# Kernel optimization log

Measured on AMD Instinct MI355X. Metric: run time of the kernel, lower is better.

## Reference

```python
import jax, jax.numpy as jnp
import numpy as np

N = 50000          # nodes (cells)
G = 1000           # input genes
E = 800000         # edges
HIDDEN = 128
HEADS = 8
C_HID = HIDDEN // HEADS   # 16 per-head channels
LATENT = 16
NEG_SLOPE = 0.2


def _gat_layer(x, src, dst, W, a_src, a_dst, b, heads, out_ch, concat):
    """PyG GATConv (shared lin for src/dst, add_self_loops=False, eval mode)."""
    n = x.shape[0]
    h = (x @ W).reshape(n, heads, out_ch)                 # [N,H,C]
    al_s = jnp.einsum('nhc,hc->nh', h, a_src)             # [N,H]
    al_d = jnp.einsum('nhc,hc->nh', h, a_dst)             # [N,H]
    logits = jax.nn.leaky_relu(al_s[src] + al_d[dst], NEG_SLOPE)  # [E,H]
    # segment softmax over destination neighborhoods
    m = jax.ops.segment_max(logits, dst, num_segments=n)  # [N,H]
    m = jnp.where(jnp.isfinite(m), m, 0.0)                # empty segments -> 0
    e = jnp.exp(logits - m[dst])                          # [E,H]
    denom = jax.ops.segment_sum(e, dst, num_segments=n)   # [N,H]
    alpha = e / (denom[dst] + 1e-16)                      # [E,H]
    msg = h[src] * alpha[:, :, None]                      # [E,H,C]
    out = jax.ops.segment_sum(msg, dst, num_segments=n)   # [N,H,C]
    out = out.reshape(n, heads * out_ch) if concat else out.mean(axis=1)
    return out + b


def setup_inputs() -> dict:
    key = jax.random.key(0)
    ks = jax.random.split(key, 16)
    x = jax.random.normal(ks[0], (N, G), dtype=jnp.float32)
    edge_index = jax.random.randint(ks[1], (2, E), 0, N, dtype=jnp.int64)

    def glorot(k, shape):
        fan_in, fan_out = shape[0], shape[-1]
        s = jnp.sqrt(6.0 / (fan_in + fan_out)).astype(jnp.float32)
        return jax.random.uniform(k, shape, jnp.float32, -s, s)

    # layer 0: G -> 8 heads x 16 (concat -> 128)
    W0 = glorot(ks[2], (G, HEADS * C_HID))
    as0 = glorot(ks[3], (HEADS, C_HID))
    ad0 = glorot(ks[4], (HEADS, C_HID))
    b0 = jnp.zeros((HEADS * C_HID,), jnp.float32)
    # layer 1: 128 -> 8 heads x 16 (concat -> 128)
    W1 = glorot(ks[5], (HIDDEN, HEADS * C_HID))
    as1 = glorot(ks[6], (HEADS, C_HID))
    ad1 = glorot(ks[7], (HEADS, C_HID))
    b1 = jnp.zeros((HEADS * C_HID,), jnp.float32)
    # layer 2: 128 -> 1 head x 16 (concat=False -> 16)
    W2 = glorot(ks[8], (HIDDEN, LATENT))
    as2 = glorot(ks[9], (1, LATENT))
    ad2 = glorot(ks[10], (1, LATENT))
    b2 = jnp.zeros((LATENT,), jnp.float32)

    return {"x": x, "edge_index": edge_index,
            "W0": W0, "as0": as0, "ad0": ad0, "b0": b0,
            "W1": W1, "as1": as1, "ad1": ad1, "b1": b1,
            "W2": W2, "as2": as2, "ad2": ad2, "b2": b2}


def reference(x, edge_index, W0, as0, ad0, b0, W1, as1, ad1, b1, W2, as2, ad2, b2):
    src, dst = edge_index[0], edge_index[1]
    h = _gat_layer(x, src, dst, W0, as0, ad0, b0, HEADS, C_HID, concat=True)
    h = jax.nn.elu(h)
    h = _gat_layer(h, src, dst, W1, as1, ad1, b1, HEADS, C_HID, concat=True)
    h = jax.nn.elu(h)
    z = _gat_layer(h, src, dst, W2, as2, ad2, b2, 1, LATENT, concat=False)
    return z
```

## Files before the change

kernel.cpp:

```cpp
#include <hip/hip_runtime.h>
#include <hip/hip_bf16.h>
#include <math.h>

#define GENES 1000

typedef __attribute__((ext_vector_type(8))) _Float16 half8;
typedef __attribute__((ext_vector_type(4))) float f32x4;
typedef __attribute__((ext_vector_type(4))) unsigned int uint4v;
typedef __attribute__((ext_vector_type(2))) unsigned int uint2v;

__device__ inline float f16lo(unsigned int v) {
  return (float)__builtin_bit_cast(_Float16, (unsigned short)(v & 0xffffu));
}
__device__ inline float f16hi(unsigned int v) {
  return (float)__builtin_bit_cast(_Float16, (unsigned short)(v >> 16));
}


__global__ void k_deg(const int* __restrict__ ei, int* __restrict__ deg, int E) {
  int e = blockIdx.x * blockDim.x + threadIdx.x;
  if (e < E) atomicAdd(&deg[ei[E + e]], 1);
}

__global__ void k_scan1(int* __restrict__ deg, int* __restrict__ ptr,
                        int* __restrict__ bsum, int n) {
  __shared__ int ws[4];
  int t = threadIdx.x, b = blockIdx.x;
  int i = b * 256 + t;
  int lane = t & 63, w = t >> 6;
  int x = 0;
  if (i < n) { x = deg[i]; deg[i] = 0; }
  #pragma unroll
  for (int d = 1; d < 64; d <<= 1) {
    int y = __shfl_up(x, d);
    if (lane >= d) x += y;
  }
  if (lane == 63) ws[w] = x;
  __syncthreads();
  if (t == 0) {
    int s = 0;
    #pragma unroll
    for (int k = 0; k < 4; ++k) { s += ws[k]; ws[k] = s; }
  }
  __syncthreads();
  int incl = x + (w ? ws[w - 1] : 0);
  if (i < n) ptr[i + 1] = incl;
  if (t == 255) bsum[b] = incl;
  if (i == 0) ptr[0] = 0;
}

__global__ void k_scan2(int* __restrict__ bsum, int nb) {
  __shared__ int ws[4];
  int t = threadIdx.x;
  int lane = t & 63, w = t >> 6;
  int v = (t < nb) ? bsum[t] : 0;
  int x = v;
  #pragma unroll
  for (int d = 1; d < 64; d <<= 1) {
    int y = __shfl_up(x, d);
    if (lane >= d) x += y;
  }
  if (lane == 63) ws[w] = x;
  __syncthreads();
  if (t == 0) {
    int s = 0;
    #pragma unroll
    for (int k = 0; k < 4; ++k) { s += ws[k]; ws[k] = s; }
  }
  __syncthreads();
  int incl = x + (w ? ws[w - 1] : 0);
  if (t < nb) bsum[t] = incl - v;
}

__global__ void k_scan3(int* __restrict__ ptr, const int* __restrict__ bsum, int n) {
  int i = blockIdx.x * 256 + threadIdx.x;
  if (i < n) ptr[i + 1] += bsum[blockIdx.x];
}

__global__ void k_scatter(const int* __restrict__ ei, const int* __restrict__ ptr,
                          int* __restrict__ cur, int* __restrict__ srcs, int E) {
  int e = blockIdx.x * blockDim.x + threadIdx.x;
  if (e >= E) return;
  int d = ei[E + e];
  int pos = ptr[d] + atomicAdd(&cur[d], 1);
  srcs[pos] = ei[e];
}


__global__ void k_wpackall(const float* __restrict__ W0, const float* __restrict__ W1,
                           const float* __restrict__ W2, unsigned short* __restrict__ P,
                           int K0) {
  int t = blockIdx.x * blockDim.x + threadIdx.x;
  if (t >= 163840) return;
  const float* W; int K, N, e;
  if (t < 131072)      { W = W0; K = K0;  N = 128; e = t; }
  else if (t < 147456) { W = W1; K = 128; N = 128; e = t - 131072; }
  else                 { W = W2; K = 128; N = 16;  e = t - 147456; }
  int s = e >> 12, rem = e & 4095;
  int q = rem >> 10, col = (rem >> 3) & 127, j = rem & 7;
  int k = s * 32 + q * 8 + j;
  float v = (k < K && col < N) ? W[(long)k * N + col] : 0.f;
  _Float16 h = (_Float16)v;
  P[t] = __builtin_bit_cast(unsigned short, h);
}


template<int HH, int NST, bool AF16, bool OF16>
__global__ __launch_bounds__(512) void k_mgemm8(
    const void* __restrict__ Ap, const unsigned short* __restrict__ Pb,
    void* __restrict__ outp, float* __restrict__ als, float* __restrict__ ald,
    const float* __restrict__ avs, const float* __restrict__ avd,
    int M, int K, int ldc) {
  __shared__ __align__(16) char lds[24576];
  char* bA0 = lds;
  char* bA1 = lds + 4096;
  char* bB0 = lds + 8192;
  char* bB1 = lds + 16384;

  int t = threadIdx.x, lane = t & 63;
  int r15 = lane & 15, q = lane >> 4;
  int wv = t >> 6;
  int wr = wv >> 1, wc = wv & 1;
  long row0 = (long)blockIdx.x * 64;

  int srow = t >> 3, sseg = t & 7;
  long arow = row0 + srow; if (arow >= M) arow = M - 1;
  const float* pa32 = (const float*)Ap + arow * (long)K;
  const unsigned short* pa16 = (const unsigned short*)Ap + arow * (long)K;

  f32x4 acc[4];
  #pragma unroll
  for (int nt = 0; nt < 4; ++nt) acc[nt] = (f32x4){0.f, 0.f, 0.f, 0.f};

  uint4v aA0, aA1, aA2;
  uint2v aH0, aH1, aH2;
  uint4v rB0, rB1;

  auto loadA = [&](int s, uint4v& r32, uint2v& r16) {
    int k0 = s * 32 + sseg * 4;
    if constexpr (AF16) {
      r16 = (k0 < K) ? *(const uint2v*)(pa16 + k0) : (uint2v){0u, 0u};
    } else {
      r32 = (k0 < K) ? *(const uint4v*)(pa32 + k0) : (uint4v){0u, 0u, 0u, 0u};
    }
  };
  auto writeA = [&](char* buf, uint4v r32, uint2v r16) {
    char* p = buf + ((sseg >> 1) * 1024 + srow * 16 + (sseg & 1) * 8);
    if constexpr (AF16) {
      *(uint2v*)p = r16;
    } else {
      float4 f = __builtin_bit_cast(float4, r32);
      uint2v h;
      h[0] = __builtin_bit_cast(unsigned int, __builtin_amdgcn_cvt_pkrtz(f.x, f.y));
      h[1] = __builtin_bit_cast(unsigned int, __builtin_amdgcn_cvt_pkrtz(f.z, f.w));
      *(uint2v*)p = h;
    }
  };
  auto ldA3 = [&](int tile) {
    int sl = tile % 3;
    if (sl == 0) loadA(tile, aA0, aH0);
    else if (sl == 1) loadA(tile, aA1, aH1);
    else loadA(tile, aA2, aH2);
  };
  auto wrA3 = [&](char* buf, int tile) {
    int sl = tile % 3;
    if (sl == 0) writeA(buf, aA0, aH0);
    else if (sl == 1) writeA(buf, aA1, aH1);
    else writeA(buf, aA2, aH2);
  };
  auto loadB = [&](int s, uint4v& r) {
    r = *(const uint4v*)(Pb + (size_t)s * 4096 + t * 8);
  };
  auto writeB = [&](char* buf, uint4v r) {
    *(uint4v*)(buf + t * 16) = r;
  };
  auto compute = [&](const char* bA, const char* bB) {
    half8 af = *(const half8*)(bA + q * 1024 + (wr * 16 + r15) * 16);
    #pragma unroll
    for (int nt = 0; nt < 4; ++nt) {
      half8 bf = *(const half8*)(bB + q * 2048 + (wc * 64 + nt * 16 + r15) * 16);
      acc[nt] = __builtin_amdgcn_mfma_f32_16x16x32_f16(af, bf, acc[nt], 0, 0, 0);
    }
  };

  ldA3(0); loadB(0, rB0);
  ldA3(1); loadB(1, rB1);
  ldA3(2);
  wrA3(bA0, 0); writeB(bB0, rB0);
  __syncthreads();

  #pragma unroll
  for (int s = 0; s < NST; s += 2) {
    if (s + 3 < NST) ldA3(s + 3);
    if (s + 2 < NST) loadB(s + 2, rB0);
    compute(bA0, bB0);
    if (s + 1 < NST) { wrA3(bA1, s + 1); writeB(bB1, rB1); }
    __syncthreads();
    if (s + 1 < NST) {
      if (s + 4 < NST) ldA3(s + 4);
      if (s + 3 < NST) loadB(s + 3, rB1);
      compute(bA1, bB1);
      if (s + 2 < NST) { wrA3(bA0, s + 2); writeB(bB0, rB0); }
      __syncthreads();
    }
  }

  long rbase = row0 + wr * 16 + q * 4;
  if constexpr (OF16) {
    unsigned short* o16 = (unsigned short*)outp;
    #pragma unroll
    for (int i = 0; i < 4; ++i) {
      long r = rbase + i;
      if (r < M) {
        #pragma unroll
        for (int nt = 0; nt < 4; ++nt) {
          int col = wc * 64 + nt * 16 + r15;
          _Float16 hv = (_Float16)acc[nt][i];
          o16[r * ldc + col] = __builtin_bit_cast(unsigned short, hv);
        }
      }
    }
  } else {
    float* o32 = (float*)outp;
    #pragma unroll
    for (int i = 0; i < 4; ++i) {
      long r = rbase + i;
      if (r < M) {
        #pragma unroll
        for (int nt = 0; nt < 4; ++nt) {
          int col = wc * 64 + nt * 16 + r15;
          if (col < ldc) o32[r * ldc + col] = acc[nt][i];
        }
      }
    }
  }
  #pragma unroll
  for (int nt = 0; nt < 4; ++nt) {
    int head = wc * 4 + nt;
    if (head < HH) {
      float cs = avs[head * 16 + r15];
      float cd = avd[head * 16 + r15];
      #pragma unroll
      for (int i = 0; i < 4; ++i) {
        float s1 = acc[nt][i] * cs;
        float s2 = acc[nt][i] * cd;
        #pragma unroll
        for (int d = 1; d < 16; d <<= 1) {
          s1 += __shfl_xor(s1, d);
          s2 += __shfl_xor(s2, d);
        }
        if (r15 == 0) {
          long r = rbase + i;
          if (r < M) { als[r * HH + head] = s1; ald[r * HH + head] = s2; }
        }
      }
    }
  }
}


__global__ void k_agg128h(const unsigned short* __restrict__ h,
                          const float* __restrict__ als, const float* __restrict__ ald,
                          const int* __restrict__ ptr, const int* __restrict__ srcs,
                          const float* __restrict__ bias,
                          unsigned short* __restrict__ out, int n) {
  int wid = (int)(((long)blockIdx.x * blockDim.x + threadIdx.x) >> 6);
  if (wid >= n) return;
  int lane = threadIdx.x & 63;
  int half = lane >> 5, l5 = lane & 31;
  int c0 = 4 * l5;
  int hB = l5 >> 2;
  int p0 = ptr[wid], deg = ptr[wid + 1] - p0;
  float aldB = ald[wid * 8 + hB];
  float a0 = 0.f, a1 = 0.f, a2 = 0.f, a3 = 0.f, dsum = 0.f;
  int j = half;
  for (; j + 6 < deg; j += 8) {
    int s0 = srcs[p0 + j],     s1 = srcs[p0 + j + 2];
    int s2 = srcs[p0 + j + 4], s3 = srcs[p0 + j + 6];
    float l0 = als[s0 * 8 + hB] + aldB;
    float l1 = als[s1 * 8 + hB] + aldB;
    float l2 = als[s2 * 8 + hB] + aldB;
    float l3 = als[s3 * 8 + hB] + aldB;
    uint2v h0 = *(const uint2v*)(h + (long)s0 * 128 + c0);
    uint2v h1 = *(const uint2v*)(h + (long)s1 * 128 + c0);
    uint2v h2 = *(const uint2v*)(h + (long)s2 * 128 + c0);
    uint2v h3 = *(const uint2v*)(h + (long)s3 * 128 + c0);
    l0 = l0 > 0.f ? l0 : 0.2f * l0;
    l1 = l1 > 0.f ? l1 : 0.2f * l1;
    l2 = l2 > 0.f ? l2 : 0.2f * l2;
    l3 = l3 > 0.f ? l3 : 0.2f * l3;
    float e0 = __expf(l0), e1 = __expf(l1), e2 = __expf(l2), e3 = __expf(l3);
    dsum += e0 + e1 + e2 + e3;
    a0 += e0 * f16lo(h0[0]) + e1 * f16lo(h1[0]) + e2 * f16lo(h2[0]) + e3 * f16lo(h3[0]);
    a1 += e0 * f16hi(h0[0]) + e1 * f16hi(h1[0]) + e2 * f16hi(h2[0]) + e3 * f16hi(h3[0]);
    a2 += e0 * f16lo(h0[1]) + e1 * f16lo(h1[1]) + e2 * f16lo(h2[1]) + e3 * f16lo(h3[1]);
    a3 += e0 * f16hi(h0[1]) + e1 * f16hi(h1[1]) + e2 * f16hi(h2[1]) + e3 * f16hi(h3[1]);
  }
  for (; j < deg; j += 2) {
    int s = srcs[p0 + j];
    float l = als[s * 8 + hB] + aldB;
    l = l > 0.f ? l : 0.2f * l;
    float e = __expf(l);
    uint2v hv = *(const uint2v*)(h + (long)s * 128 + c0);
    dsum += e;
    a0 += e * f16lo(hv[0]);
    a1 += e * f16hi(hv[0]);
    a2 += e * f16lo(hv[1]);
    a3 += e * f16hi(hv[1]);
  }
  a0 += __shfl_xor(a0, 32);
  a1 += __shfl_xor(a1, 32);
  a2 += __shfl_xor(a2, 32);
  a3 += __shfl_xor(a3, 32);
  dsum += __shfl_xor(dsum, 32);
  if (half == 0) {
    float inv = 1.f / (dsum + 1e-16f);
    float o0 = a0 * inv + bias[c0];
    float o1 = a1 * inv + bias[c0 + 1];
    float o2 = a2 * inv + bias[c0 + 2];
    float o3 = a3 * inv + bias[c0 + 3];
    o0 = o0 > 0.f ? o0 : (__expf(o0) - 1.f);
    o1 = o1 > 0.f ? o1 : (__expf(o1) - 1.f);
    o2 = o2 > 0.f ? o2 : (__expf(o2) - 1.f);
    o3 = o3 > 0.f ? o3 : (__expf(o3) - 1.f);
    uint2v po;
    po[0] = __builtin_bit_cast(unsigned int, __builtin_amdgcn_cvt_pkrtz(o0, o1));
    po[1] = __builtin_bit_cast(unsigned int, __builtin_amdgcn_cvt_pkrtz(o2, o3));
    *(uint2v*)(out + (long)wid * 128 + c0) = po;
  }
}


__global__ void k_agg16(const float* __restrict__ h, const float* __restrict__ als,
                        const float* __restrict__ ald, const int* __restrict__ ptr,
                        const int* __restrict__ srcs, const float* __restrict__ bias,
                        float* __restrict__ out, int n, int lda) {
  int wid = (int)(((long)blockIdx.x * blockDim.x + threadIdx.x) >> 6);
  if (wid >= n) return;
  int lane = threadIdx.x & 63;
  int p0 = ptr[wid], deg = ptr[wid + 1] - p0;
  float aldv = ald[wid];
  int g = lane >> 4, c = lane & 15;
  float acc = 0.f, dsum = 0.f;
  int j = g;
  for (; j + 12 < deg; j += 16) {
    int s0 = srcs[p0 + j],     s1 = srcs[p0 + j + 4];
    int s2 = srcs[p0 + j + 8], s3 = srcs[p0 + j + 12];
    float l0 = als[s0] + aldv, l1 = als[s1] + aldv;
    float l2 = als[s2] + aldv, l3 = als[s3] + aldv;
    float h0 = h[(long)s0 * lda + c], h1 = h[(long)s1 * lda + c];
    float h2 = h[(long)s2 * lda + c], h3 = h[(long)s3 * lda + c];
    l0 = l0 > 0.f ? l0 : 0.2f * l0;
    l1 = l1 > 0.f ? l1 : 0.2f * l1;
    l2 = l2 > 0.f ? l2 : 0.2f * l2;
    l3 = l3 > 0.f ? l3 : 0.2f * l3;
    float e0 = __expf(l0), e1 = __expf(l1), e2 = __expf(l2), e3 = __expf(l3);
    dsum += e0 + e1 + e2 + e3;
    acc += e0 * h0 + e1 * h1 + e2 * h2 + e3 * h3;
  }
  for (; j < deg; j += 4) {
    int s = srcs[p0 + j];
    float l = als[s] + aldv;
    l = l > 0.f ? l : 0.2f * l;
    float e = __expf(l);
    dsum += e;
    acc += e * h[(long)s * lda + c];
  }
  #pragma unroll
  for (int d = 16; d < 64; d <<= 1) {
    acc += __shfl_xor(acc, d);
    dsum += __shfl_xor(dsum, d);
  }
  if (lane < 16)
    out[(long)wid * 16 + lane] = acc / (dsum + 1e-16f) + bias[lane];
}


extern "C" void kernel_launch(void* const* d_in, const int* in_sizes, int n_in,
                              void* d_out, int out_size, void* d_ws, size_t ws_size,
                              hipStream_t stream) {
  const float* x  = (const float*)d_in[0];
  const int*   ei = (const int*)d_in[1];
  const float* W0 = (const float*)d_in[2];
  const float* as0= (const float*)d_in[3];
  const float* ad0= (const float*)d_in[4];
  const float* b0 = (const float*)d_in[5];
  const float* W1 = (const float*)d_in[6];
  const float* as1= (const float*)d_in[7];
  const float* ad1= (const float*)d_in[8];
  const float* b1 = (const float*)d_in[9];
  const float* W2 = (const float*)d_in[10];
  const float* as2= (const float*)d_in[11];
  const float* ad2= (const float*)d_in[12];
  const float* b2 = (const float*)d_in[13];
  float* out = (float*)d_out;

  int E = in_sizes[1] / 2;
  int n = in_sizes[0] / GENES;

  char* ws = (char*)d_ws;
  size_t off = 0;
  auto alloc = [&](size_t bytes) {
    void* p = ws + off;
    off = (off + bytes + 255) & ~(size_t)255;
    return p;
  };
  int* ptr   = (int*)alloc((size_t)(n + 1) * sizeof(int));
  int* cur   = (int*)alloc((size_t)n * sizeof(int));
  int* bsum  = (int*)alloc(512 * sizeof(int));
  int* srcs  = (int*)alloc((size_t)E * sizeof(int));
  unsigned short* Ah = (unsigned short*)alloc((size_t)n * 128 * sizeof(unsigned short));
  unsigned short* Bh = (unsigned short*)alloc((size_t)n * 128 * sizeof(unsigned short));
  float* A2  = (float*)alloc((size_t)n * 16 * sizeof(float));
  float* als = (float*)alloc((size_t)n * 8 * sizeof(float));
  float* ald = (float*)alloc((size_t)n * 8 * sizeof(float));
  unsigned short* P = (unsigned short*)alloc((size_t)163840 * sizeof(unsigned short));
  unsigned short* P0 = P;
  unsigned short* P1 = P + 131072;
  unsigned short* P2 = P + 147456;

  int eb = (E + 255) / 256;
  int nb = (n + 255) / 256;
  hipMemsetAsync(cur, 0, (size_t)n * sizeof(int), stream);
  k_deg<<<eb, 256, 0, stream>>>(ei, cur, E);
  k_scan1<<<nb, 256, 0, stream>>>(cur, ptr, bsum, n);
  k_scan2<<<1, 256, 0, stream>>>(bsum, nb);
  k_scan3<<<nb, 256, 0, stream>>>(ptr, bsum, n);
  k_scatter<<<eb, 256, 0, stream>>>(ei, ptr, cur, srcs, E);
  k_wpackall<<<640, 256, 0, stream>>>(W0, W1, W2, P, GENES);

  int mgb  = (n + 63) / 64;
  int aggb = (int)(((long)n * 64 + 255) / 256);

  k_mgemm8<8, 32, false, true><<<mgb, 512, 0, stream>>>(
      x, P0, Ah, als, ald, as0, ad0, n, GENES, 128);
  k_agg128h<<<aggb, 256, 0, stream>>>(Ah, als, ald, ptr, srcs, b0, Bh, n);

  k_mgemm8<8, 4, true, true><<<mgb, 512, 0, stream>>>(
      Bh, P1, Ah, als, ald, as1, ad1, n, 128, 128);
  k_agg128h<<<aggb, 256, 0, stream>>>(Ah, als, ald, ptr, srcs, b1, Bh, n);

  k_mgemm8<1, 4, true, false><<<mgb, 512, 0, stream>>>(
      Bh, P2, A2, als, ald, as2, ad2, n, 128, 16);
  k_agg16<<<aggb, 256, 0, stream>>>(A2, als, ald, ptr, srcs, b2, out, n, 16);
}
```

Before: 275.8 us.

## Load GEMM A fragments straight from global into registers, bypassing LDS

The GEMM kernel now loads each lane's A-operand fragment directly from global memory into registers and converts it to fp16 in place. The A tiles are no longer staged through shared memory, and only B tiles stay double-buffered in LDS. The loop now advances one K-step per iteration and uses a custom barrier that waits only on LDS counters, which removes the A LDS writes and reads and shrinks shared memory. In exchange it drops the k<K bounds check on A: the padded K tail reads past each row, into the next row or past the end of the buffer. This relies on the zero-padded packed weights to cancel those values.

Result: slower. 282.0 us (+2.2%).

```diff
diff --git a/kernel.cpp b/kernel.cpp
--- a/kernel.cpp
+++ b/kernel.cpp
@@ -14,6 +14,17 @@
 }
 __device__ inline float f16hi(unsigned int v) {
   return (float)__builtin_bit_cast(_Float16, (unsigned short)(v >> 16));
+}
+__device__ inline unsigned int pk(float a, float b) {
+  return __builtin_bit_cast(unsigned int, __builtin_amdgcn_cvt_pkrtz(a, b));
+}
+
+__device__ inline void lds_barrier() {
+  __builtin_amdgcn_sched_barrier(0);
+  asm volatile("s_waitcnt lgkmcnt(0)" ::: "memory");
+  __builtin_amdgcn_sched_barrier(0);
+  __builtin_amdgcn_s_barrier();
+  __builtin_amdgcn_sched_barrier(0);
 }
 
 
@@ -106,16 +117,12 @@
 
 
 template<int HH, int NST, bool AF16, bool OF16>
-__global__ __launch_bounds__(512) void k_mgemm8(
+__global__ __launch_bounds__(512) void k_mgemm10(
     const void* __restrict__ Ap, const unsigned short* __restrict__ Pb,
     void* __restrict__ outp, float* __restrict__ als, float* __restrict__ ald,
     const float* __restrict__ avs, const float* __restrict__ avd,
     int M, int K, int ldc) {
-  __shared__ __align__(16) char lds[24576];
-  char* bA0 = lds;
-  char* bA1 = lds + 4096;
-  char* bB0 = lds + 8192;
-  char* bB1 = lds + 16384;
+  __shared__ __align__(16) char lds[16384];
 
   int t = threadIdx.x, lane = t & 63;
   int r15 = lane & 15, q = lane >> 4;
@@ -123,85 +130,73 @@
   int wr = wv >> 1, wc = wv & 1;
   long row0 = (long)blockIdx.x * 64;
 
-  int srow = t >> 3, sseg = t & 7;
-  long arow = row0 + srow; if (arow >= M) arow = M - 1;
-  const float* pa32 = (const float*)Ap + arow * (long)K;
-  const unsigned short* pa16 = (const unsigned short*)Ap + arow * (long)K;
+  long arow = row0 + wr * 16 + r15; if (arow >= M) arow = M - 1;
+  const float* pa32 = (const float*)Ap + arow * (long)K + q * 8;
+  const unsigned short* pa16 = (const unsigned short*)Ap + arow * (long)K + q * 8;
+  const char* pB = (const char*)Pb + t * 16;
 
   f32x4 acc[4];
   #pragma unroll
   for (int nt = 0; nt < 4; ++nt) acc[nt] = (f32x4){0.f, 0.f, 0.f, 0.f};
 
-  uint4v aA0, aA1, aA2;
-  uint2v aH0, aH1, aH2;
-  uint4v rB0, rB1;
-
-  auto loadA = [&](int s, uint4v& r32, uint2v& r16) {
-    int k0 = s * 32 + sseg * 4;
+  uint4v a0lo, a0hi, a1lo, a1hi;
+  uint4v bs0, bs1;
+
+  auto issueA = [&](int s, int slot) {
     if constexpr (AF16) {
-      r16 = (k0 < K) ? *(const uint2v*)(pa16 + k0) : (uint2v){0u, 0u};
+      if (slot == 0) a0lo = *(const uint4v*)(pa16 + s * 32);
+      else           a1lo = *(const uint4v*)(pa16 + s * 32);
     } else {
-      r32 = (k0 < K) ? *(const uint4v*)(pa32 + k0) : (uint4v){0u, 0u, 0u, 0u};
+      if (slot == 0) {
+        a0lo = *(const uint4v*)(pa32 + s * 32);
+        a0hi = *(const uint4v*)(pa32 + s * 32 + 4);
+      } else {
+        a1lo = *(const uint4v*)(pa32 + s * 32);
+        a1hi = *(const uint4v*)(pa32 + s * 32 + 4);
+      }
     }
   };
-  auto writeA = [&](char* buf, uint4v r32, uint2v r16) {
-    char* p = buf + ((sseg >> 1) * 1024 + srow * 16 + (sseg & 1) * 8);
+  auto issueB = [&](int s, int slot) {
+    if (slot == 0) bs0 = *(const uint4v*)(pB + (size_t)s * 8192);
+    else           bs1 = *(const uint4v*)(pB + (size_t)s * 8192);
+  };
+  auto writeB = [&](int buf, int slot) {
+    *(uint4v*)(lds + buf * 8192 + t * 16) = (slot == 0) ? bs0 : bs1;
+  };
+  auto mkfrag = [&](int slot) -> half8 {
     if constexpr (AF16) {
-      *(uint2v*)p = r16;
+      return __builtin_bit_cast(half8, slot == 0 ? a0lo : a1lo);
     } else {
-      float4 f = __builtin_bit_cast(float4, r32);
-      uint2v h;
-      h[0] = __builtin_bit_cast(unsigned int, __builtin_amdgcn_cvt_pkrtz(f.x, f.y));
-      h[1] = __builtin_bit_cast(unsigned int, __builtin_amdgcn_cvt_pkrtz(f.z, f.w));
-      *(uint2v*)p = h;
+      float4 lo = __builtin_bit_cast(float4, slot == 0 ? a0lo : a1lo);
+      float4 hi = __builtin_bit_cast(float4, slot == 0 ? a0hi : a1hi);
+      uint4v au;
+      au[0] = pk(lo.x, lo.y); au[1] = pk(lo.z, lo.w);
+      au[2] = pk(hi.x, hi.y); au[3] = pk(hi.z, hi.w);
+      return __builtin_bit_cast(half8, au);
     }
   };
-  auto ldA3 = [&](int tile) {
-    int sl = tile % 3;
-    if (sl == 0) loadA(tile, aA0, aH0);
-    else if (sl == 1) loadA(tile, aA1, aH1);
-    else loadA(tile, aA2, aH2);
-  };
-  auto wrA3 = [&](char* buf, int tile) {
-    int sl = tile % 3;
-    if (sl == 0) writeA(buf, aA0, aH0);
-    else if (sl == 1) writeA(buf, aA1, aH1);
-    else writeA(buf, aA2, aH2);
-  };
-  auto loadB = [&](int s, uint4v& r) {
-    r = *(const uint4v*)(Pb + (size_t)s * 4096 + t * 8);
-  };
-  auto writeB = [&](char* buf, uint4v r) {
-    *(uint4v*)(buf + t * 16) = r;
-  };
-  auto compute = [&](const char* bA, const char* bB) {
-    half8 af = *(const half8*)(bA + q * 1024 + (wr * 16 + r15) * 16);
+
+  issueB(0, 0);
+  if (NST > 1) issueB(1, 1);
+  issueA(0, 0);
+  writeB(0, 0);
+  lds_barrier();
+
+  #pragma unroll
+  for (int s = 0; s < NST; ++s) {
+    const int sl = s & 1;
+    if (s + 2 < NST) issueB(s + 2, sl);
+    if (s + 1 < NST) issueA(s + 1, (s + 1) & 1);
+    half8 af = mkfrag(sl);
     #pragma unroll
     for (int nt = 0; nt < 4; ++nt) {
-      half8 bf = *(const half8*)(bB + q * 2048 + (wc * 64 + nt * 16 + r15) * 16);
+      half8 bf = *(const half8*)(lds + sl * 8192 + q * 2048 +
+                                 (wc * 64 + nt * 16 + r15) * 16);
       acc[nt] = __builtin_amdgcn_mfma_f32_16x16x32_f16(af, bf, acc[nt], 0, 0, 0);
     }
-  };
-
-  ldA3(0); loadB(0, rB0);
-  ldA3(1); loadB(1, rB1);
-  ldA3(2);
-  wrA3(bA0, 0); writeB(bB0, rB0);
-  __syncthreads();
-
-  #pragma unroll
-  for (int s = 0; s < NST; s += 2) {
-    if (s + 3 < NST) ldA3(s + 3);
-    if (s + 2 < NST) loadB(s + 2, rB0);
-    compute(bA0, bB0);
-    if (s + 1 < NST) { wrA3(bA1, s + 1); writeB(bB1, rB1); }
-    __syncthreads();
     if (s + 1 < NST) {
-      if (s + 4 < NST) ldA3(s + 4);
-      if (s + 3 < NST) loadB(s + 3, rB1);
-      compute(bA1, bB1);
-      if (s + 2 < NST) { wrA3(bA0, s + 2); writeB(bB0, rB0); }
-      __syncthreads();
+      writeB((s + 1) & 1, (s + 1) & 1);
+      lds_barrier();
     }
   }
 
@@ -432,15 +427,15 @@
   int mgb  = (n + 63) / 64;
   int aggb = (int)(((long)n * 64 + 255) / 256);
 
-  k_mgemm8<8, 32, false, true><<<mgb, 512, 0, stream>>>(
+  k_mgemm10<8, 32, false, true><<<mgb, 512, 0, stream>>>(
       x, P0, Ah, als, ald, as0, ad0, n, GENES, 128);
   k_agg128h<<<aggb, 256, 0, stream>>>(Ah, als, ald, ptr, srcs, b0, Bh, n);
 
-  k_mgemm8<8, 4, true, true><<<mgb, 512, 0, stream>>>(
+  k_mgemm10<8, 4, true, true><<<mgb, 512, 0, stream>>>(
       Bh, P1, Ah, als, ald, as1, ad1, n, 128, 128);
   k_agg128h<<<aggb, 256, 0, stream>>>(Ah, als, ald, ptr, srcs, b1, Bh, n);
 
-  k_mgemm8<1, 4, true, false><<<mgb, 512, 0, stream>>>(
+  k_mgemm10<1, 4, true, false><<<mgb, 512, 0, stream>>>(
       Bh, P2, A2, als, ald, as2, ad2, n, 128, 16);
   k_agg16<<<aggb, 256, 0, stream>>>(A2, als, ald, ptr, srcs, b2, out, n, 16);
 }
```
